# Optimization experiments

Measured on AMD Instinct MI355X. Metric: run time of the kernel, lower is better.

Reference implementation:

```python
import math
import jax, jax.numpy as jnp
import numpy as np

NEG_INF = -1e9


def maximum_path(neg_cent, text_len, spec_len):
    """Monotonic alignment search (VITS). neg_cent: [B, Ty(spec), Tx(text)].
    Returns hard path [B, Ty, Tx] (float32, 0/1)."""
    B, Ty, Tx = neg_cent.shape
    xs = jnp.arange(Tx)

    # Forward DP over spec frames y; carry = best cumulative value per text pos x.
    def fwd_step(value, inp):
        y, score = inp  # score: [B, Tx]
        diag = jnp.pad(value[:, :-1], ((0, 0), (1, 0)), constant_values=NEG_INF)
        d = diag > value  # move-diagonally indicator for backtracking
        new = score + jnp.maximum(value, diag)
        new = jnp.where(y == 0, jnp.where(xs == 0, score, NEG_INF), new)
        return new, d

    init = jnp.full((B, Tx), NEG_INF, dtype=neg_cent.dtype)
    _, dirs = jax.lax.scan(fwd_step, init,
                           (jnp.arange(Ty), jnp.swapaxes(neg_cent, 0, 1)))
    # dirs: [Ty, B, Tx] bool; dirs[y] compares row y-1 values (as in cython MAS).

    # Backtrack from (spec_len-1, text_len-1) down to y=0.
    def bwd_step(index, inp):
        y, d_row = inp  # index: [B] int32, d_row: [B, Tx]
        active = y < spec_len  # [B]
        row = jnp.where(active[:, None],
                        jax.nn.one_hot(index, Tx, dtype=jnp.float32), 0.0)
        d_at = jnp.take_along_axis(d_row, index[:, None], axis=1)[:, 0]
        move = (index != 0) & ((index == y) | d_at)
        index = jnp.where(active & move, index - 1, index)
        return index, row

    init_idx = text_len - 1
    _, path = jax.lax.scan(bwd_step, init_idx, (jnp.arange(Ty), dirs),
                           reverse=True)
    return jnp.swapaxes(path, 0, 1)  # [B, Ty, Tx]


def setup_inputs() -> dict:
    key = jax.random.key(0)
    ks = jax.random.split(key, 6)
    B, C, Tx, Ty = 8, 192, 512, 2048
    z_p = jax.random.normal(ks[0], (B, C, Ty), dtype=jnp.float32)
    m_p = jax.random.normal(ks[1], (B, C, Tx), dtype=jnp.float32)
    logs_p = 0.1 * jax.random.normal(ks[2], (B, C, Tx), dtype=jnp.float32)
    logs_q = 0.1 * jax.random.normal(ks[3], (B, C, Ty), dtype=jnp.float32)
    text_len = jax.random.randint(ks[4], (B,), Tx * 3 // 4, Tx + 1)
    spec_len = jax.random.randint(ks[5], (B,), Ty * 3 // 4, Ty + 1)
    text_mask = (jnp.arange(Tx)[None, :] < text_len[:, None]).astype(jnp.float32)[:, None, :]
    spec_mask = (jnp.arange(Ty)[None, :] < spec_len[:, None]).astype(jnp.float32)[:, None, :]
    return {"z_p": z_p, "m_p": m_p, "logs_p": logs_p, "logs_q": logs_q,
            "text_mask": text_mask, "spec_mask": spec_mask}


def reference(z_p, m_p, logs_p, logs_q, text_mask, spec_mask):
    text_len = jnp.sum(text_mask, axis=(1, 2)).astype(jnp.int32)  # [B]
    spec_len = jnp.sum(spec_mask, axis=(1, 2)).astype(jnp.int32)  # [B]

    # ---- search_path: neg log-likelihood grid [B, T_spec, T_text] ----
    s_p_sq_r = jnp.exp(-2.0 * logs_p)  # [B, C, Tx]
    nc1 = jnp.sum(-0.5 * math.log(2 * math.pi) - logs_p, axis=1, keepdims=True)  # [B,1,Tx]
    nc2 = jnp.einsum('bct,bcx->btx', -0.5 * z_p * z_p, s_p_sq_r)
    nc3 = jnp.einsum('bct,bcx->btx', z_p, m_p * s_p_sq_r)
    nc4 = jnp.sum(-0.5 * m_p * m_p * s_p_sq_r, axis=1, keepdims=True)  # [B,1,Tx]
    neg_cent = nc1 + nc2 + nc3 + nc4  # [B, Ty, Tx]

    MAS_path = maximum_path(neg_cent, text_len, spec_len)  # [B, Ty, Tx]

    # ---- gather-combine text stats onto spec frames ----
    m_p_a = jnp.einsum('btx,bcx->bct', MAS_path, m_p)      # [B, C, Ty]
    logs_p_a = jnp.einsum('btx,bcx->bct', MAS_path, logs_p)

    # ---- KL divergence loss (VITS) ----
    kl = logs_p_a - logs_q - 0.5 \
        + 0.5 * jnp.square(z_p - m_p_a) * jnp.exp(-2.0 * logs_p_a)
    loss_kl = jnp.sum(kl * spec_mask) / jnp.sum(spec_mask)

    duration = jnp.sum(MAS_path, axis=1)[:, None, :]  # [B, 1, Tx]
    return MAS_path[:, None], m_p_a, logs_p_a, loss_kl, duration
```

## Files before the change

### kernel.cpp

```cpp
#include <hip/hip_runtime.h>
#include <cstdint>
#include <cstddef>

#define BB 8
#define CC 192
#define TXX 512
#define TYY 2048
#define NG_MAX (TYY / 8)

#define NEG_INF (-1e9f)
#define HALF_LOG_2PI 0.9189385332046727f

#define O1 8388608
#define O2 11534336
#define O3 14680064
#define O4 14680065

#define WS_NEG   0
#define WS_S     33554432
#define WS_MSR   36700160
#define WS_BIAS  39845888
#define WS_DIRS  39862272
#define WS_IDX   40910848
#define WS_LENS  40976384
#define WS_PART  40976448

typedef float f32x4 __attribute__((ext_vector_type(4)));

__global__ void k_zero(float* __restrict__ out) {
    int64_t i = (int64_t)blockIdx.x * blockDim.x + threadIdx.x;
    const int64_t n4 = (int64_t)BB * TYY * TXX / 4;
    float4 z4 = make_float4(0.f, 0.f, 0.f, 0.f);
    float4* p4 = (float4*)out;
    for (int64_t k = i; k < n4; k += (int64_t)gridDim.x * blockDim.x) p4[k] = z4;
    if (i < BB * TXX) out[O4 + i] = 0.0f;
}

__global__ void k_prep(const float* __restrict__ logs_p, const float* __restrict__ m_p,
                       float* __restrict__ s, float* __restrict__ msr) {
    int i = blockIdx.x * blockDim.x + threadIdx.x;
    float lp = logs_p[i], m = m_p[i];
    float sv = expf(-2.0f * lp);
    s[i] = sv;
    msr[i] = m * sv;
}

__global__ void k_bias(const float* __restrict__ logs_p, const float* __restrict__ m_p,
                       const float* __restrict__ msr, float* __restrict__ bias) {
    int i = blockIdx.x * blockDim.x + threadIdx.x;
    int b = i >> 9, x = i & (TXX - 1);
    size_t base = (size_t)b * CC * TXX + x;
    const float* lpb = logs_p + base;
    const float* mb  = m_p + base;
    const float* msb = msr + base;
    float acc = 0.f;
#pragma unroll 8
    for (int c = 0; c < CC; ++c)
        acc += -HALF_LOG_2PI - lpb[(size_t)c * TXX] - 0.5f * mb[(size_t)c * TXX] * msb[(size_t)c * TXX];
    bias[i] = acc;
}

__global__ void k_len(const float* __restrict__ tmask, const float* __restrict__ smask,
                      int* __restrict__ lens) {
    __shared__ float red[256];
    int b = blockIdx.x, tid = threadIdx.x;
    float ts = 0.f;
    for (int i = tid; i < TXX; i += 256) ts += tmask[b * TXX + i];
    red[tid] = ts; __syncthreads();
    for (int s = 128; s > 0; s >>= 1) { if (tid < s) red[tid] += red[tid + s]; __syncthreads(); }
    if (tid == 0) lens[b] = (int)(red[0] + 0.5f);
    __syncthreads();
    float ss = 0.f;
    for (int i = tid; i < TYY; i += 256) ss += smask[b * TYY + i];
    red[tid] = ss; __syncthreads();
    for (int s = 128; s > 0; s >>= 1) { if (tid < s) red[tid] += red[tid + s]; __syncthreads(); }
    if (tid == 0) lens[8 + b] = (int)(red[0] + 0.5f);
}

__global__ __launch_bounds__(256) void k_gemm(const float* __restrict__ z,
                                              const float* __restrict__ msr,
                                              const float* __restrict__ sarr,
                                              const float* __restrict__ bias,
                                              const int* __restrict__ lens,
                                              float* __restrict__ neg) {
    int x0 = blockIdx.x * 64, t0 = blockIdx.y * 64, b = blockIdx.z;
    if (x0 >= lens[b] || t0 >= lens[8 + b]) return;

    __shared__ float Zs[16][68], Ms[16][68], Ss[16][68];
    int tid = threadIdx.x;
    int tx = tid & 15, ty = tid >> 4;
    const float* zb = z    + (size_t)b * CC * TYY;
    const float* mb = msr  + (size_t)b * CC * TXX;
    const float* sb = sarr + (size_t)b * CC * TXX;
    int lr = tid >> 4, lc = (tid & 15) * 4;
    float acc[4][4] = {};
    for (int k0 = 0; k0 < CC; k0 += 16) {
        float4 zv = *(const float4*)(zb + (size_t)(k0 + lr) * TYY + t0 + lc);
        float4 mv = *(const float4*)(mb + (size_t)(k0 + lr) * TXX + x0 + lc);
        float4 sv = *(const float4*)(sb + (size_t)(k0 + lr) * TXX + x0 + lc);
        __syncthreads();
        *(float4*)&Zs[lr][lc] = zv;
        *(float4*)&Ms[lr][lc] = mv;
        *(float4*)&Ss[lr][lc] = sv;
        __syncthreads();
#pragma unroll
        for (int k = 0; k < 16; ++k) {
            float4 a4  = *(const float4*)&Zs[k][ty * 4];
            float4 bm4 = *(const float4*)&Ms[k][tx * 4];
            float4 bs4 = *(const float4*)&Ss[k][tx * 4];
            float av[4]  = {a4.x, a4.y, a4.z, a4.w};
            float bmv[4] = {bm4.x, bm4.y, bm4.z, bm4.w};
            float bsv[4] = {bs4.x, bs4.y, bs4.z, bs4.w};
#pragma unroll
            for (int i2 = 0; i2 < 4; ++i2) {
                float a2 = -0.5f * av[i2] * av[i2];
#pragma unroll
                for (int j = 0; j < 4; ++j)
                    acc[i2][j] += av[i2] * bmv[j] + a2 * bsv[j];
            }
        }
    }
    float4 b4 = *(const float4*)(bias + b * TXX + x0 + tx * 4);
    float bv[4] = {b4.x, b4.y, b4.z, b4.w};
#pragma unroll
    for (int i2 = 0; i2 < 4; ++i2) {
        int t = t0 + ty * 4 + i2;
        float4 o;
        o.x = acc[i2][0] + bv[0]; o.y = acc[i2][1] + bv[1];
        o.z = acc[i2][2] + bv[2]; o.w = acc[i2][3] + bv[3];
        *(float4*)(neg + ((size_t)b * TYY + t) * TXX + x0 + tx * 4) = o;
    }
}

#define WAIT_VM(N) do {                                                   \
    asm volatile("s_waitcnt vmcnt(" #N ")" ::: "memory");                 \
    __builtin_amdgcn_sched_barrier(0);                                    \
} while (0)

#define GLDS(GP, LP)                                                      \
    __builtin_amdgcn_global_load_lds(                                     \
        (__attribute__((address_space(1))) void*)(GP),                    \
        (__attribute__((address_space(3))) void*)(LP), 16, 0, 0)

#define STAGE(G) do {                                                     \
    const char* gb_ = gsrc + (size_t)(G) * 16384;                         \
    char* lb_ = ring + (((G) & 3) * 16384);                               \
    _Pragma("unroll")                                                     \
    for (int c_ = 0; c_ < 16; ++c_)                                       \
        GLDS(gb_ + c_ * 1024, lb_ + c_ * 1024);                           \
} while (0)

#define LOADQ(SL)                                                         \
    const char* sp_ = (SL) + lbase;                                       \
    f32x4 q0l = *(const f32x4*)(sp_ + sw0);                               \
    f32x4 q0h = *(const f32x4*)(sp_ + sw1);                               \
    f32x4 q1l = *(const f32x4*)(sp_ + 2048 + sw0);                        \
    f32x4 q1h = *(const f32x4*)(sp_ + 2048 + sw1);                        \
    f32x4 q2l = *(const f32x4*)(sp_ + 4096 + sw0);                        \
    f32x4 q2h = *(const f32x4*)(sp_ + 4096 + sw1);                        \
    f32x4 q3l = *(const f32x4*)(sp_ + 6144 + sw0);                        \
    f32x4 q3h = *(const f32x4*)(sp_ + 6144 + sw1);                        \
    f32x4 q4l = *(const f32x4*)(sp_ + 8192 + sw0);                        \
    f32x4 q4h = *(const f32x4*)(sp_ + 8192 + sw1);                        \
    f32x4 q5l = *(const f32x4*)(sp_ + 10240 + sw0);                       \
    f32x4 q5h = *(const f32x4*)(sp_ + 10240 + sw1);                       \
    f32x4 q6l = *(const f32x4*)(sp_ + 12288 + sw0);                       \
    f32x4 q6h = *(const f32x4*)(sp_ + 12288 + sw1);                       \
    f32x4 q7l = *(const f32x4*)(sp_ + 14336 + sw0);                       \
    f32x4 q7h = *(const f32x4*)(sp_ + 14336 + sw1);                       \
    __builtin_amdgcn_sched_barrier(0);

#define DPROW(QL, QH, R) do {                                                 \
    float s0_ = QL[0], s1_ = QL[1], s2_ = QL[2], s3_ = QL[3];                 \
    float s4_ = QH[0], s5_ = QH[1], s6_ = QH[2], s7_ = QH[3];                 \
    unsigned d_ = 0;                                                          \
    float pl_ = __int_as_float(__builtin_amdgcn_update_dpp(                   \
        0, __float_as_int(v[7]), 0x138, 0xF, 0xF, false));                    \
    if (lane == 0) pl_ = NEG_INF;                                             \
    float n0_ = s0_ + fmaxf(v[0], pl_);  if (pl_  > v[0]) d_ |= 1u;           \
    float n1_ = s1_ + fmaxf(v[1], v[0]); if (v[0] > v[1]) d_ |= 2u;           \
    float n2_ = s2_ + fmaxf(v[2], v[1]); if (v[1] > v[2]) d_ |= 4u;           \
    float n3_ = s3_ + fmaxf(v[3], v[2]); if (v[2] > v[3]) d_ |= 8u;           \
    float n4_ = s4_ + fmaxf(v[4], v[3]); if (v[3] > v[4]) d_ |= 16u;          \
    float n5_ = s5_ + fmaxf(v[5], v[4]); if (v[4] > v[5]) d_ |= 32u;          \
    float n6_ = s6_ + fmaxf(v[6], v[5]); if (v[5] > v[6]) d_ |= 64u;          \
    float n7_ = s7_ + fmaxf(v[7], v[6]); if (v[6] > v[7]) d_ |= 128u;         \
    v[0] = n0_; v[1] = n1_; v[2] = n2_; v[3] = n3_;                           \
    v[4] = n4_; v[5] = n5_; v[6] = n6_; v[7] = n7_;                           \
    acc |= d_ << (((R) & 3) * 8);                                             \
} while (0)

__global__ __launch_bounds__(64, 1) void k_fwd(const float* __restrict__ neg,
                                               const int* __restrict__ lens,
                                               uint32_t* __restrict__ dirs) {
    __shared__ __align__(16) char ring[4 * 16384];
    int b = blockIdx.x, lane = threadIdx.x;
    unsigned gsw = ((unsigned)lane * 16u) ^ ((((unsigned)lane >> 3) & 1u) << 4);
    const char* gsrc = (const char*)(neg + (size_t)b * TYY * TXX) + gsw;
    unsigned lbase = (unsigned)lane * 32u;
    unsigned sw0 = (((unsigned)lane >> 2) & 1u) << 4;
    unsigned sw1 = sw0 ^ 16u;
    uint32_t* db32 = dirs + (size_t)b * (TYY / 4) * 64;
    int slen = lens[8 + b];
    int ng = (slen + 7) >> 3;

    float v[8];
#pragma unroll
    for (int j = 0; j < 8; ++j) v[j] = NEG_INF;
    unsigned acc = 0;

    STAGE(0); STAGE(1); STAGE(2); STAGE(3);
    WAIT_VM(48);

    {
        LOADQ(ring);
        unsigned fm0 = (lane == 0) ? 0x08040201u : 0u;
        unsigned fm1 = (lane == 0) ? 0x80402010u : 0u;
        if (lane == 0) v[0] = q0l[0];
        DPROW(q1l, q1h, 1); DPROW(q2l, q2h, 2); DPROW(q3l, q3h, 3);
        uint32_t* dp_ = db32 + lane;
        dp_[0] = acc | fm0; acc = 0;
        DPROW(q4l, q4h, 4); DPROW(q5l, q5h, 5);
        DPROW(q6l, q6h, 6); DPROW(q7l, q7h, 7);
        dp_[64] = acc | fm1; acc = 0;
    }

#pragma unroll 1
    for (int g = 1; g < ng; ++g) {
        if (g + 3 < ng)      { STAGE(g + 3); WAIT_VM(48); }
        else if (g + 2 < ng) { WAIT_VM(32); }
        else if (g + 1 < ng) { WAIT_VM(16); }
        else                 { WAIT_VM(0);  }
        const char* sl = ring + ((g & 3) * 16384);
        LOADQ(sl);
        unsigned fm0 = (lane == g) ? 0x08040201u : 0u;
        unsigned fm1 = (lane == g) ? 0x80402010u : 0u;
        uint32_t* dp_ = db32 + ((unsigned)g << 7) + lane;
        DPROW(q0l, q0h, 0); DPROW(q1l, q1h, 1);
        DPROW(q2l, q2h, 2); DPROW(q3l, q3h, 3);
        dp_[0] = acc | fm0; acc = 0;
        DPROW(q4l, q4h, 4); DPROW(q5l, q5h, 5);
        DPROW(q6l, q6h, 6); DPROW(q7l, q7h, 7);
        dp_[64] = acc | fm1; acc = 0;
    }
}

__global__ __launch_bounds__(64, 1) void k_bwd(const int* __restrict__ lens,
                                               const uint32_t* __restrict__ dirs,
                                               int* __restrict__ idx_map) {
    int b = blockIdx.x, lane = threadIdx.x;
    const uint32_t* db32 = dirs + (size_t)b * (TYY / 4) * 64;
    int tlen = lens[b], slen = lens[8 + b];

    int idx = tlen - 1;
    int y0 = slen - 1;
    while (y0 >= 0) {
        int nsteps = (y0 + 1 < 32) ? y0 + 1 : 32;
        int y = y0 - lane;
        int yy = (y < 0) ? 0 : y;
        int w0 = (idx >> 5) - 1;
        if (w0 < 0) w0 = 0;
        if (w0 > 14) w0 = 14;
        int qrow = (yy >> 2) * 64;
        int byteoff = (yy & 3) * 8;
        uint32_t lo = 0, hi = 0;
        if (lane < 32) {
#pragma unroll
            for (int k = 0; k < 4; ++k)
                lo |= ((db32[qrow + 4 * w0 + k] >> byteoff) & 0xffu) << (8 * k);
#pragma unroll
            for (int k = 0; k < 4; ++k)
                hi |= ((db32[qrow + 4 * w0 + 4 + k] >> byteoff) & 0xffu) << (8 * k);
        }
        int base = w0 << 5;
        int cap = 0;
#pragma unroll
        for (int j = 0; j < 32; ++j) {
            if (lane == j) cap = idx;
            uint32_t l = (uint32_t)__builtin_amdgcn_readlane((int)lo, j);
            uint32_t h = (uint32_t)__builtin_amdgcn_readlane((int)hi, j);
            int bp = idx - base;
            uint32_t word = (bp & 32) ? h : l;
            int bit = (int)((word >> (bp & 31)) & 1u);
            int move = (int)(idx != 0) & bit;
            idx -= move;
        }
        if (lane < nsteps) idx_map[b * TYY + (y0 - lane)] = cap;
        y0 -= 32;
    }
}

__global__ void k_scatter(const int* __restrict__ lens, const int* __restrict__ idx_map,
                          float* __restrict__ out) {
    int i = blockIdx.x * blockDim.x + threadIdx.x;
    int b = i >> 11, y = i & (TYY - 1);
    if (y < lens[8 + b]) {
        int x = idx_map[i];
        out[(size_t)i * TXX + x] = 1.0f;
        atomicAdd(&out[O4 + b * TXX + x], 1.0f);
    }
}

__global__ __launch_bounds__(256) void k_gather(const float* __restrict__ z_p,
                                                const float* __restrict__ m_p,
                                                const float* __restrict__ logs_p,
                                                const float* __restrict__ logs_q,
                                                const int* __restrict__ lens,
                                                const int* __restrict__ idx_map,
                                                float* __restrict__ out,
                                                float* __restrict__ partials) {
    const int S = BB * CC * TYY / 4;
    int base = blockIdx.x * 256 + threadIdx.x;
    float klsum = 0.f;
#pragma unroll
    for (int r = 0; r < 4; ++r) {
        int i = base + r * S;
        int t = i & (TYY - 1);
        int bc = i >> 11;
        int b = bc / CC;
        float ma = 0.f, la = 0.f;
        if (t < lens[8 + b]) {
            int x = idx_map[b * TYY + t];
            size_t off = (size_t)bc * TXX + x;
            ma = m_p[off];
            la = logs_p[off];
            float zv = z_p[i], lq = logs_q[i];
            float dz = zv - ma;
            klsum += la - lq - 0.5f + 0.5f * dz * dz * expf(-2.0f * la);
        }
        out[O1 + i] = ma;
        out[O2 + i] = la;
    }
    for (int o = 32; o > 0; o >>= 1) klsum += __shfl_down(klsum, o);
    __shared__ float red[4];
    if ((threadIdx.x & 63) == 0) red[threadIdx.x >> 6] = klsum;
    __syncthreads();
    if (threadIdx.x == 0) partials[blockIdx.x] = red[0] + red[1] + red[2] + red[3];
}

__global__ void k_final(const float* __restrict__ partials, const int* __restrict__ lens,
                        float* __restrict__ out) {
    float s = 0.f;
    for (int i = threadIdx.x; i < 3072; i += 256) s += partials[i];
    for (int o = 32; o > 0; o >>= 1) s += __shfl_down(s, o);
    __shared__ float red[4];
    if ((threadIdx.x & 63) == 0) red[threadIdx.x >> 6] = s;
    __syncthreads();
    if (threadIdx.x == 0) {
        float tot = 0.f;
        for (int b = 0; b < 8; ++b) tot += (float)lens[8 + b];
        out[O3] = (red[0] + red[1] + red[2] + red[3]) / tot;
    }
}

extern "C" void kernel_launch(void* const* d_in, const int* in_sizes, int n_in,
                              void* d_out, int out_size, void* d_ws, size_t ws_size,
                              hipStream_t stream) {
    const float* z_p    = (const float*)d_in[0];
    const float* m_p    = (const float*)d_in[1];
    const float* logs_p = (const float*)d_in[2];
    const float* logs_q = (const float*)d_in[3];
    const float* tmask  = (const float*)d_in[4];
    const float* smask  = (const float*)d_in[5];
    float* out = (float*)d_out;
    char* ws = (char*)d_ws;

    float*    neg      = (float*)(ws + WS_NEG);
    float*    sarr     = (float*)(ws + WS_S);
    float*    msr      = (float*)(ws + WS_MSR);
    float*    bias     = (float*)(ws + WS_BIAS);
    uint32_t* dirs     = (uint32_t*)(ws + WS_DIRS);
    int*      idx_map  = (int*)(ws + WS_IDX);
    int*      lens     = (int*)(ws + WS_LENS);
    float*    partials = (float*)(ws + WS_PART);

    hipLaunchKernelGGL(k_zero,    dim3(2048),      dim3(256), 0, stream, out);
    hipLaunchKernelGGL(k_prep,    dim3(3072),      dim3(256), 0, stream, logs_p, m_p, sarr, msr);
    hipLaunchKernelGGL(k_bias,    dim3(16),        dim3(256), 0, stream, logs_p, m_p, msr, bias);
    hipLaunchKernelGGL(k_len,     dim3(8),         dim3(256), 0, stream, tmask, smask, lens);
    hipLaunchKernelGGL(k_gemm,    dim3(8, 32, 8),  dim3(256), 0, stream, z_p, msr, sarr, bias, lens, neg);
    hipLaunchKernelGGL(k_fwd,     dim3(8),         dim3(64),  0, stream, neg, lens, dirs);
    hipLaunchKernelGGL(k_bwd,     dim3(8),         dim3(64),  0, stream, lens, dirs, idx_map);
    hipLaunchKernelGGL(k_scatter, dim3(64),        dim3(256), 0, stream, lens, idx_map, out);
    hipLaunchKernelGGL(k_gather,  dim3(3072),      dim3(256), 0, stream, z_p, m_p, logs_p, logs_q,
                       lens, idx_map, out, partials);
    hipLaunchKernelGGL(k_final,   dim3(1),         dim3(256), 0, stream, partials, lens, out);
}
```

Before: 591.2 us.

## Software-pipeline LDS reads in forward DP and fuse backtrack into forward kernel

The forward DP kernel now double-buffers register tiles: while one 8-row group is computed, the next group's LDS reads are already issued. The async global-to-LDS prefetch also moves one stage deeper, with adjusted vmcnt waits. The backtrack is folded into the same kernel after the forward pass, which removes a launch and a round trip of the direction bits through L2. The kernel also drops the lane-0 select by passing NEG_INF as the DPP old value, and k_bias gets a different launch shape. The cost is roughly double the vector register use and hand-tuned waitcnt values that must match the number of loads in flight.

Result: no change. 591.5 us (+0.0%).

```diff
diff --git a/kernel.cpp b/kernel.cpp
--- a/kernel.cpp
+++ b/kernel.cpp
@@ -137,6 +137,11 @@
     __builtin_amdgcn_sched_barrier(0);                                    \
 } while (0)
 
+#define LGKM0 do {                                                        \
+    asm volatile("s_waitcnt lgkmcnt(0)" ::: "memory");                    \
+    __builtin_amdgcn_sched_barrier(0);                                    \
+} while (0)
+
 #define GLDS(GP, LP)                                                      \
     __builtin_amdgcn_global_load_lds(                                     \
         (__attribute__((address_space(1))) void*)(GP),                    \
@@ -150,33 +155,32 @@
         GLDS(gb_ + c_ * 1024, lb_ + c_ * 1024);                           \
 } while (0)
 
-#define LOADQ(SL)                                                         \
-    const char* sp_ = (SL) + lbase;                                       \
-    f32x4 q0l = *(const f32x4*)(sp_ + sw0);                               \
-    f32x4 q0h = *(const f32x4*)(sp_ + sw1);                               \
-    f32x4 q1l = *(const f32x4*)(sp_ + 2048 + sw0);                        \
-    f32x4 q1h = *(const f32x4*)(sp_ + 2048 + sw1);                        \
-    f32x4 q2l = *(const f32x4*)(sp_ + 4096 + sw0);                        \
-    f32x4 q2h = *(const f32x4*)(sp_ + 4096 + sw1);                        \
-    f32x4 q3l = *(const f32x4*)(sp_ + 6144 + sw0);                        \
-    f32x4 q3h = *(const f32x4*)(sp_ + 6144 + sw1);                        \
-    f32x4 q4l = *(const f32x4*)(sp_ + 8192 + sw0);                        \
-    f32x4 q4h = *(const f32x4*)(sp_ + 8192 + sw1);                        \
-    f32x4 q5l = *(const f32x4*)(sp_ + 10240 + sw0);                       \
-    f32x4 q5h = *(const f32x4*)(sp_ + 10240 + sw1);                       \
-    f32x4 q6l = *(const f32x4*)(sp_ + 12288 + sw0);                       \
-    f32x4 q6h = *(const f32x4*)(sp_ + 12288 + sw1);                       \
-    f32x4 q7l = *(const f32x4*)(sp_ + 14336 + sw0);                       \
-    f32x4 q7h = *(const f32x4*)(sp_ + 14336 + sw1);                       \
-    __builtin_amdgcn_sched_barrier(0);
+#define LOADQ(P, SLP) do {                                                \
+    const char* sp_ = (const char*)(SLP) + lbase;                         \
+    P##0l = *(const f32x4*)(sp_ + sw0);                                   \
+    P##0h = *(const f32x4*)(sp_ + sw1);                                   \
+    P##1l = *(const f32x4*)(sp_ + 2048 + sw0);                            \
+    P##1h = *(const f32x4*)(sp_ + 2048 + sw1);                            \
+    P##2l = *(const f32x4*)(sp_ + 4096 + sw0);                            \
+    P##2h = *(const f32x4*)(sp_ + 4096 + sw1);                            \
+    P##3l = *(const f32x4*)(sp_ + 6144 + sw0);                            \
+    P##3h = *(const f32x4*)(sp_ + 6144 + sw1);                            \
+    P##4l = *(const f32x4*)(sp_ + 8192 + sw0);                            \
+    P##4h = *(const f32x4*)(sp_ + 8192 + sw1);                            \
+    P##5l = *(const f32x4*)(sp_ + 10240 + sw0);                           \
+    P##5h = *(const f32x4*)(sp_ + 10240 + sw1);                           \
+    P##6l = *(const f32x4*)(sp_ + 12288 + sw0);                           \
+    P##6h = *(const f32x4*)(sp_ + 12288 + sw1);                           \
+    P##7l = *(const f32x4*)(sp_ + 14336 + sw0);                           \
+    P##7h = *(const f32x4*)(sp_ + 14336 + sw1);                           \
+} while (0)
 
 #define DPROW(QL, QH, R) do {                                                 \
     float s0_ = QL[0], s1_ = QL[1], s2_ = QL[2], s3_ = QL[3];                 \
     float s4_ = QH[0], s5_ = QH[1], s6_ = QH[2], s7_ = QH[3];                 \
     unsigned d_ = 0;                                                          \
     float pl_ = __int_as_float(__builtin_amdgcn_update_dpp(                   \
-        0, __float_as_int(v[7]), 0x138, 0xF, 0xF, false));                    \
-    if (lane == 0) pl_ = NEG_INF;                                             \
+        ninf_i, __float_as_int(v[7]), 0x138, 0xF, 0xF, false));               \
     float n0_ = s0_ + fmaxf(v[0], pl_);  if (pl_  > v[0]) d_ |= 1u;           \
     float n1_ = s1_ + fmaxf(v[1], v[0]); if (v[0] > v[1]) d_ |= 2u;           \
     float n2_ = s2_ + fmaxf(v[2], v[1]); if (v[1] > v[2]) d_ |= 4u;           \
@@ -190,9 +194,34 @@
     acc |= d_ << (((R) & 3) * 8);                                             \
 } while (0)
 
+#define DPROWS(P, G) do {                                                     \
+    unsigned fm0_ = (lane == (G)) ? 0x08040201u : 0u;                         \
+    unsigned fm1_ = (lane == (G)) ? 0x80402010u : 0u;                         \
+    uint32_t* dp_ = db32 + ((unsigned)(G) << 7) + lane;                       \
+    DPROW(P##0l, P##0h, 0); DPROW(P##1l, P##1h, 1);                           \
+    DPROW(P##2l, P##2h, 2); DPROW(P##3l, P##3h, 3);                           \
+    dp_[0] = acc | fm0_; acc = 0;                                             \
+    DPROW(P##4l, P##4h, 4); DPROW(P##5l, P##5h, 5);                           \
+    DPROW(P##6l, P##6h, 6); DPROW(P##7l, P##7h, 7);                           \
+    dp_[64] = acc | fm1_; acc = 0;                                            \
+} while (0)
+
+#define PHASE(CURP, NXTP) do {                                                \
+    if (g == ng - 1) { DPROWS(CURP, g); goto fwd_done; }                      \
+    if (g + 3 < ng) { if (g >= 3) { WAIT_VM(38); } else { WAIT_VM(32); } }    \
+    else if (g + 2 < ng) { WAIT_VM(22); }                                     \
+    else { WAIT_VM(6); }                                                      \
+    LGKM0;                                                                    \
+    if (g + 4 < ng) STAGE(g + 4);                                             \
+    LOADQ(NXTP, ring + (((g + 1) & 3) * 16384));                              \
+    DPROWS(CURP, g);                                                          \
+    ++g;                                                                      \
+} while (0)
+
 __global__ __launch_bounds__(64, 1) void k_fwd(const float* __restrict__ neg,
                                                const int* __restrict__ lens,
-                                               uint32_t* __restrict__ dirs) {
+                                               uint32_t* __restrict__ dirs,
+                                               int* __restrict__ idx_map) {
     __shared__ __align__(16) char ring[4 * 16384];
     int b = blockIdx.x, lane = threadIdx.x;
     unsigned gsw = ((unsigned)lane * 16u) ^ ((((unsigned)lane >> 3) & 1u) << 4);
@@ -203,90 +232,82 @@
     uint32_t* db32 = dirs + (size_t)b * (TYY / 4) * 64;
     int slen = lens[8 + b];
     int ng = (slen + 7) >> 3;
+    int ninf_i = __float_as_int(NEG_INF);
 
     float v[8];
 #pragma unroll
     for (int j = 0; j < 8; ++j) v[j] = NEG_INF;
     unsigned acc = 0;
 
+    f32x4 a0l, a0h, a1l, a1h, a2l, a2h, a3l, a3h;
+    f32x4 a4l, a4h, a5l, a5h, a6l, a6h, a7l, a7h;
+    f32x4 b0l, b0h, b1l, b1h, b2l, b2h, b3l, b3h;
+    f32x4 b4l, b4h, b5l, b5h, b6l, b6h, b7l, b7h;
+
     STAGE(0); STAGE(1); STAGE(2); STAGE(3);
     WAIT_VM(48);
-
+    LOADQ(a, ring);
+
+    WAIT_VM(32);
+    LGKM0;
+    STAGE(4);
+    LOADQ(b, ring + 16384);
     {
-        LOADQ(ring);
-        unsigned fm0 = (lane == 0) ? 0x08040201u : 0u;
-        unsigned fm1 = (lane == 0) ? 0x80402010u : 0u;
-        if (lane == 0) v[0] = q0l[0];
-        DPROW(q1l, q1h, 1); DPROW(q2l, q2h, 2); DPROW(q3l, q3h, 3);
+        if (lane == 0) v[0] = a0l[0];
+        unsigned fm0_ = (lane == 0) ? 0x08040201u : 0u;
+        unsigned fm1_ = (lane == 0) ? 0x80402010u : 0u;
         uint32_t* dp_ = db32 + lane;
-        dp_[0] = acc | fm0; acc = 0;
-        DPROW(q4l, q4h, 4); DPROW(q5l, q5h, 5);
-        DPROW(q6l, q6h, 6); DPROW(q7l, q7h, 7);
-        dp_[64] = acc | fm1; acc = 0;
-    }
-
-#pragma unroll 1
-    for (int g = 1; g < ng; ++g) {
-        if (g + 3 < ng)      { STAGE(g + 3); WAIT_VM(48); }
-        else if (g + 2 < ng) { WAIT_VM(32); }
-        else if (g + 1 < ng) { WAIT_VM(16); }
-        else                 { WAIT_VM(0);  }
-        const char* sl = ring + ((g & 3) * 16384);
-        LOADQ(sl);
-        unsigned fm0 = (lane == g) ? 0x08040201u : 0u;
-        unsigned fm1 = (lane == g) ? 0x80402010u : 0u;
-        uint32_t* dp_ = db32 + ((unsigned)g << 7) + lane;
-        DPROW(q0l, q0h, 0); DPROW(q1l, q1h, 1);
-        DPROW(q2l, q2h, 2); DPROW(q3l, q3h, 3);
-        dp_[0] = acc | fm0; acc = 0;
-        DPROW(q4l, q4h, 4); DPROW(q5l, q5h, 5);
-        DPROW(q6l, q6h, 6); DPROW(q7l, q7h, 7);
-        dp_[64] = acc | fm1; acc = 0;
-    }
-}
-
-__global__ __launch_bounds__(64, 1) void k_bwd(const int* __restrict__ lens,
-                                               const uint32_t* __restrict__ dirs,
-                                               int* __restrict__ idx_map) {
-    int b = blockIdx.x, lane = threadIdx.x;
-    const uint32_t* db32 = dirs + (size_t)b * (TYY / 4) * 64;
-    int tlen = lens[b], slen = lens[8 + b];
-
-    int idx = tlen - 1;
-    int y0 = slen - 1;
-    while (y0 >= 0) {
-        int nsteps = (y0 + 1 < 32) ? y0 + 1 : 32;
-        int y = y0 - lane;
-        int yy = (y < 0) ? 0 : y;
-        int w0 = (idx >> 5) - 1;
-        if (w0 < 0) w0 = 0;
-        if (w0 > 14) w0 = 14;
-        int qrow = (yy >> 2) * 64;
-        int byteoff = (yy & 3) * 8;
-        uint32_t lo = 0, hi = 0;
-        if (lane < 32) {
-#pragma unroll
-            for (int k = 0; k < 4; ++k)
-                lo |= ((db32[qrow + 4 * w0 + k] >> byteoff) & 0xffu) << (8 * k);
-#pragma unroll
-            for (int k = 0; k < 4; ++k)
-                hi |= ((db32[qrow + 4 * w0 + 4 + k] >> byteoff) & 0xffu) << (8 * k);
+        DPROW(a1l, a1h, 1); DPROW(a2l, a2h, 2); DPROW(a3l, a3h, 3);
+        dp_[0] = acc | fm0_; acc = 0;
+        DPROW(a4l, a4h, 4); DPROW(a5l, a5h, 5);
+        DPROW(a6l, a6h, 6); DPROW(a7l, a7h, 7);
+        dp_[64] = acc | fm1_; acc = 0;
+    }
+    int g = 1;
+    while (1) {
+        PHASE(b, a);
+        PHASE(a, b);
+    }
+fwd_done:
+    WAIT_VM(0);
+    {
+        int tlen = lens[b];
+        int idx = tlen - 1;
+        int y0 = slen - 1;
+        while (y0 >= 0) {
+            int nsteps = (y0 + 1 < 32) ? y0 + 1 : 32;
+            int y = y0 - lane;
+            int yy = (y < 0) ? 0 : y;
+            int w0 = (idx >> 5) - 1;
+            if (w0 < 0) w0 = 0;
+            if (w0 > 14) w0 = 14;
+            int qrow = (yy >> 2) * 64;
+            int byteoff = (yy & 3) * 8;
+            uint32_t lo = 0, hi = 0;
+            if (lane < 32) {
+#pragma unroll
+                for (int k = 0; k < 4; ++k)
+                    lo |= ((db32[qrow + 4 * w0 + k] >> byteoff) & 0xffu) << (8 * k);
+#pragma unroll
+                for (int k = 0; k < 4; ++k)
+                    hi |= ((db32[qrow + 4 * w0 + 4 + k] >> byteoff) & 0xffu) << (8 * k);
+            }
+            int base = w0 << 5;
+            int cap = 0;
+#pragma unroll
+            for (int j = 0; j < 32; ++j) {
+                if (lane == j) cap = idx;
+                uint32_t l = (uint32_t)__builtin_amdgcn_readlane((int)lo, j);
+                uint32_t h = (uint32_t)__builtin_amdgcn_readlane((int)hi, j);
+                int bp = idx - base;
+                uint32_t word = (bp & 32) ? h : l;
+                int bit = (int)((word >> (bp & 31)) & 1u);
+                int move = (int)(idx != 0) & bit;
+                idx -= move;
+            }
+            if (lane < nsteps) idx_map[b * TYY + (y0 - lane)] = cap;
+            y0 -= 32;
         }
-        int base = w0 << 5;
-        int cap = 0;
-#pragma unroll
-        for (int j = 0; j < 32; ++j) {
-            if (lane == j) cap = idx;
-            uint32_t l = (uint32_t)__builtin_amdgcn_readlane((int)lo, j);
-            uint32_t h = (uint32_t)__builtin_amdgcn_readlane((int)hi, j);
-            int bp = idx - base;
-            uint32_t word = (bp & 32) ? h : l;
-            int bit = (int)((word >> (bp & 31)) & 1u);
-            int move = (int)(idx != 0) & bit;
-            idx -= move;
-        }
-        if (lane < nsteps) idx_map[b * TYY + (y0 - lane)] = cap;
-        y0 -= 32;
     }
 }
 
@@ -376,11 +397,10 @@
 
     hipLaunchKernelGGL(k_zero,    dim3(2048),      dim3(256), 0, stream, out);
     hipLaunchKernelGGL(k_prep,    dim3(3072),      dim3(256), 0, stream, logs_p, m_p, sarr, msr);
-    hipLaunchKernelGGL(k_bias,    dim3(16),        dim3(256), 0, stream, logs_p, m_p, msr, bias);
+    hipLaunchKernelGGL(k_bias,    dim3(64),        dim3(64),  0, stream, logs_p, m_p, msr, bias);
     hipLaunchKernelGGL(k_len,     dim3(8),         dim3(256), 0, stream, tmask, smask, lens);
     hipLaunchKernelGGL(k_gemm,    dim3(8, 32, 8),  dim3(256), 0, stream, z_p, msr, sarr, bias, lens, neg);
-    hipLaunchKernelGGL(k_fwd,     dim3(8),         dim3(64),  0, stream, neg, lens, dirs);
-    hipLaunchKernelGGL(k_bwd,     dim3(8),         dim3(64),  0, stream, lens, dirs, idx_map);
+    hipLaunchKernelGGL(k_fwd,     dim3(8),         dim3(64),  0, stream, neg, lens, dirs, idx_map);
     hipLaunchKernelGGL(k_scatter, dim3(64),        dim3(256), 0, stream, lens, idx_map, out);
     hipLaunchKernelGGL(k_gather,  dim3(3072),      dim3(256), 0, stream, z_p, m_p, logs_p, logs_q,
                        lens, idx_map, out, partials);
```
